# Performance work log

Hardware: AMD Instinct MI355X
Metric: run time of the kernel (lower is better)

## Reference

```python
import jax, jax.numpy as jnp
import numpy as np

B, C, H, W = 2, 128, 64, 64


def setup_inputs() -> dict:
    key = jax.random.key(0)
    ks = jax.random.split(key, 16)
    s = 1.0 / np.sqrt(C)
    d = {
        "x": jax.random.normal(ks[0], (B, C, H, W), jnp.float32),
        "y": jax.random.normal(ks[1], (B, C, H, W), jnp.float32),
    }
    names = ["qr", "qi", "kr", "ki", "vr", "vi"]
    for i, n in enumerate(names):
        d["W" + n] = jax.random.normal(ks[2 + 2 * i], (C, C), jnp.float32) * s
        d["b" + n] = jax.random.normal(ks[3 + 2 * i], (C,), jnp.float32) * s
    return d


def _lin(t, Wt, bt):
    # t: [b, n, c]; torch Linear: t @ W^T + b
    return jnp.einsum("bnc,dc->bnd", t, Wt) + bt


def reference(x, y, Wqr, bqr, Wqi, bqi, Wkr, bkr, Wki, bki, Wvr, bvr, Wvi, bvi):
    b, c, h, w = x.shape
    xf = jnp.fft.fft2(x)  # over last two axes (h, w)
    yf = jnp.fft.fft2(y)
    # b c h w -> b (h w) c
    def flat(t):
        return t.transpose(0, 2, 3, 1).reshape(b, h * w, c)
    xr, xi = flat(xf.real), flat(xf.imag)
    yr, yi = flat(yf.real), flat(yf.imag)

    Qr = _lin(xr, Wqr, bqr) - _lin(xi, Wqi, bqi)
    Qi = _lin(xi, Wqr, bqr) + _lin(xr, Wqi, bqi)
    Kr = _lin(yr, Wkr, bkr) - _lin(yi, Wki, bki)
    Ki = _lin(yi, Wkr, bkr) + _lin(yr, Wki, bki)
    Vr = _lin(yr, Wvr, bvr) - _lin(yi, Wvi, bvi)
    Vi = _lin(yi, Wvr, bvr) + _lin(yr, Wvi, bvi)

    sr = jnp.einsum("bnc,bmc->bnm", Qr, Kr) - jnp.einsum("bnc,bmc->bnm", Qi, Ki)
    si = jnp.einsum("bnc,bmc->bnm", Qr, Ki) + jnp.einsum("bnc,bmc->bnm", Qi, Kr)
    scores = jnp.sqrt(sr * sr + si * si + 1e-8)
    attn = jax.nn.softmax(scores, axis=-1)

    out_r = jnp.einsum("bnm,bmc->bnc", attn, Vr)
    out_i = jnp.einsum("bnm,bmc->bnc", attn, Vi)
    out_c = jax.lax.complex(out_r, out_i)
    # b (h w) c -> b c h w
    out_c = out_c.reshape(b, h, w, c).transpose(0, 3, 1, 2)
    return jnp.fft.ifft2(out_c).real
```

## Files before the change

kernel.cpp:

```cpp
#include <hip/hip_runtime.h>
#include <math.h>


#define PI2 6.283185307179586f

typedef __attribute__((ext_vector_type(8))) short short8;
typedef __attribute__((ext_vector_type(4))) float f32x4;

#define MFMA16(A,B,C) __builtin_amdgcn_mfma_f32_16x16x32_bf16((A),(B),(C),0,0,0)

__device__ inline unsigned short f2bf(float x){
  union{float f; unsigned int u;} a; a.f = x;
  unsigned int r = (a.u + 0x7fffu + ((a.u>>16)&1u)) >> 16;
  return (unsigned short)r;
}
__device__ inline float bf2f(unsigned short h){
  union{unsigned int u; float f;} a; a.u = ((unsigned int)h)<<16; return a.f;
}
__device__ inline short8 neg8(short8 x){
  union{short8 v; unsigned int u[4];} a; a.v = x;
  a.u[0]^=0x80008000u; a.u[1]^=0x80008000u; a.u[2]^=0x80008000u; a.u[3]^=0x80008000u;
  return a.v;
}
__device__ inline void gload_lds16(const void* g, void* lds){
  __builtin_amdgcn_global_load_lds((const __attribute__((address_space(1))) unsigned int*)g,
                                   (__attribute__((address_space(3))) unsigned int*)lds,
                                   16, 0, 0);
}

__global__ __launch_bounds__(256) void dft2_fwd_kernel(
    const float* __restrict__ x, const float* __restrict__ y,
    float* __restrict__ xr, float* __restrict__ xi,
    float* __restrict__ yr, float* __restrict__ yi)
{
  __shared__ float Xs[4096];
  __shared__ float Tr[4096], Ti[4096];
  __shared__ float twc[64], tws[64];
  int blk = blockIdx.x;
  const float* src; float *outr, *outi;
  int plane;
  if (blk < 256) { src = x; outr = xr; outi = xi; plane = blk; }
  else           { src = y; outr = yr; outi = yi; plane = blk - 256; }
  int b = plane >> 7, c = plane & 127;
  int t = threadIdx.x;
  if (t < 64) {
    float ang = -PI2 * (float)t / 64.0f;
    twc[t] = cosf(ang); tws[t] = sinf(ang);
  }
  const float* p = src + ((size_t)plane << 12);
  for (int i = t; i < 4096; i += 256) Xs[i] = p[i];
  __syncthreads();
  for (int j = 0; j < 16; j++) {
    int o = t + 256 * j; int h = o >> 6, wp = o & 63;
    float ar = 0.f, ai = 0.f;
    for (int w = 0; w < 64; w++) {
      int k = (w * wp) & 63;
      float v = Xs[h * 64 + w];
      ar = fmaf(v, twc[k], ar);
      ai = fmaf(v, tws[k], ai);
    }
    Tr[h * 64 + wp] = ar; Ti[h * 64 + wp] = ai;
  }
  __syncthreads();
  size_t ob = ((size_t)b * 4096) * 128 + c;
  for (int j = 0; j < 16; j++) {
    int o = t + 256 * j; int hp = o >> 6, wp = o & 63;
    float ar = 0.f, ai = 0.f;
    for (int h = 0; h < 64; h++) {
      int k = (h * hp) & 63;
      float cr = twc[k], ci = tws[k];
      float tr = Tr[h * 64 + wp], ti = Ti[h * 64 + wp];
      ar += tr * cr - ti * ci;
      ai += tr * ci + ti * cr;
    }
    int n = (hp << 6) + wp;
    outr[ob + (size_t)n * 128] = ar;
    outi[ob + (size_t)n * 128] = ai;
  }
}

__global__ __launch_bounds__(256) void proj_kernel(
    const float* __restrict__ xr, const float* __restrict__ xi,
    const float* __restrict__ yr, const float* __restrict__ yi,
    const float* __restrict__ Wqr, const float* __restrict__ bqr,
    const float* __restrict__ Wqi, const float* __restrict__ bqi,
    const float* __restrict__ Wkr, const float* __restrict__ bkr,
    const float* __restrict__ Wki, const float* __restrict__ bki,
    const float* __restrict__ Wvr, const float* __restrict__ bvr,
    const float* __restrict__ Wvi, const float* __restrict__ bvi,
    unsigned short* __restrict__ FQ, unsigned short* __restrict__ FK,
    unsigned short* __restrict__ FV)
{
  __shared__ float Asr[64 * 33], Asi[64 * 33], Wsr[128 * 33], Wsi[128 * 33];
  int nt = blockIdx.x, lin = blockIdx.y, b = blockIdx.z;
  const float *ar, *ai, *Wr, *Wi, *br_, *bi_;
  unsigned short* F;
  if (lin == 0)      { ar = xr; ai = xi; Wr = Wqr; Wi = Wqi; br_ = bqr; bi_ = bqi; F = FQ; }
  else if (lin == 1) { ar = yr; ai = yi; Wr = Wkr; Wi = Wki; br_ = bkr; bi_ = bki; F = FK; }
  else               { ar = yr; ai = yi; Wr = Wvr; Wi = Wvi; br_ = bvr; bi_ = bvi; F = FV; }
  int t = threadIdx.x; int td = t & 15, tn = t >> 4;
  int n0 = nt * 64;
  size_t abase = (size_t)b * 4096 * 128 + (size_t)n0 * 128;
  const size_t PS = (size_t)2 * 4096 * 128;
  float accr[4][8] = {}, acci[4][8] = {};
  for (int kk = 0; kk < 4; kk++) {
    __syncthreads();
    for (int idx = t; idx < 64 * 32; idx += 256) {
      int r = idx >> 5, ccol = idx & 31;
      Asr[r * 33 + ccol] = ar[abase + (size_t)r * 128 + kk * 32 + ccol];
      Asi[r * 33 + ccol] = ai[abase + (size_t)r * 128 + kk * 32 + ccol];
    }
    for (int idx = t; idx < 128 * 32; idx += 256) {
      int r = idx >> 5, ccol = idx & 31;
      Wsr[r * 33 + ccol] = Wr[(size_t)r * 128 + kk * 32 + ccol];
      Wsi[r * 33 + ccol] = Wi[(size_t)r * 128 + kk * 32 + ccol];
    }
    __syncthreads();
    for (int k = 0; k < 32; k++) {
      float a_r[4], a_i[4], w_r[8], w_i[8];
      #pragma unroll
      for (int i = 0; i < 4; i++) {
        a_r[i] = Asr[(tn * 4 + i) * 33 + k];
        a_i[i] = Asi[(tn * 4 + i) * 33 + k];
      }
      #pragma unroll
      for (int jj = 0; jj < 8; jj++) {
        w_r[jj] = Wsr[(td + 16 * jj) * 33 + k];
        w_i[jj] = Wsi[(td + 16 * jj) * 33 + k];
      }
      #pragma unroll
      for (int i = 0; i < 4; i++)
        #pragma unroll
        for (int jj = 0; jj < 8; jj++) {
          accr[i][jj] += a_r[i] * w_r[jj] - a_i[i] * w_i[jj];
          acci[i][jj] += a_i[i] * w_r[jj] + a_r[i] * w_i[jj];
        }
    }
  }
  for (int jj = 0; jj < 8; jj++) {
    int d = td + 16 * jj;
    float brd = br_[d], bid = bi_[d];
    #pragma unroll
    for (int i = 0; i < 4; i++) {
      int n = n0 + tn * 4 + i;
      float cr = accr[i][jj] + (brd - bid);
      float ci = acci[i][jj] + (brd + bid);
      size_t base = ((size_t)b * 4096 + n) * 128 + d;
      if (lin <= 1) {
        unsigned short rh = f2bf(cr); unsigned short rl = f2bf(cr - bf2f(rh));
        unsigned short ih = f2bf(ci); unsigned short il = f2bf(ci - bf2f(ih));
        F[0 * PS + base] = rh;
        F[1 * PS + base] = rl;
        F[2 * PS + base] = ih;
        F[3 * PS + base] = il;
      } else {
        F[0 * PS + base] = f2bf(cr);
        F[1 * PS + base] = f2bf(ci);
      }
    }
  }
}

__global__ __launch_bounds__(256) void kpack_kernel(
    const unsigned short* __restrict__ F, unsigned short* __restrict__ Kpk)
{
  int blk = blockIdx.x;
  int b = blk >> 6, mt = blk & 63;
  int t = threadIdx.x;
  size_t obase = (size_t)blk * 4096;
  #pragma unroll
  for (int k = 0; k < 16; k++) {
    int idx = t + 256 * k;
    int l = idx & 63, s = (idx >> 6) & 3, tml = (idx >> 8) & 3, a = idx >> 10;
    int n = mt * 64 + tml * 16 + (l & 15);
    int c0 = 32 * s + 8 * (l >> 4);
    const short8 v = *(const short8*)(F + (((size_t)(a * 2 + b) * 4096 + n) * 128 + c0));
    *(short8*)(Kpk + (obase + idx) * 8) = v;
  }
}

__global__ __launch_bounds__(256) void vpack_kernel(
    const unsigned short* __restrict__ F, unsigned short* __restrict__ Vpk)
{
  __shared__ unsigned short Vs[2 * 32 * 128];
  int blk = blockIdx.x;
  int b = blk >> 7, sm = blk & 127;
  int t = threadIdx.x;
  const size_t PS = (size_t)2 * 4096 * 128;
  #pragma unroll
  for (int p = 0; p < 2; p++) {
    #pragma unroll
    for (int k = 0; k < 2; k++) {
      int idx8 = t + 256 * k;
      int nn = idx8 >> 4, d0 = (idx8 & 15) * 8;
      const short8 v = *(const short8*)(F + p * PS + ((size_t)(b * 4096 + sm * 32 + nn)) * 128 + d0);
      *(short8*)(Vs + (p * 32 + nn) * 128 + d0) = v;
    }
  }
  __syncthreads();
  size_t obase = (size_t)blk * 1024;
  #pragma unroll
  for (int k = 0; k < 4; k++) {
    int idx = t + 256 * k;
    int lv = idx & 63, tc = idx >> 6;
    int vh = tc >> 3;
    int d = (tc & 7) * 16 + (lv & 15);
    int nb = (lv >> 4) * 8;
    short8 v;
    #pragma unroll
    for (int j = 0; j < 8; j++)
      v[j] = (short)Vs[(vh * 32 + nb + j) * 128 + d];
    *(short8*)(Vpk + (obase + idx) * 8) = v;
  }
}

__global__ __launch_bounds__(256, 2) void attn_mfma_kernel(
    const unsigned short* __restrict__ FQ, const short* __restrict__ Kpk,
    const short* __restrict__ Vpk,
    float* __restrict__ Or_, float* __restrict__ Oi_)
{
  __shared__ __align__(16) short Klds[32768];
  __shared__ __align__(16) short Pfrag[16 * 72];
  __shared__ __align__(16) float rmax[16][4];

  const int bi = blockIdx.x;
  const int xg = bi & 7;
  const int b = xg >> 2;
  const int qt2 = (bi >> 3) * 4 + (xg & 3);
  const int t = threadIdx.x;
  const int ms = t >> 6, l = t & 63;
  const int g = l >> 4, c = l & 15;

  const size_t PS = (size_t)2 * 4096 * 128;
  short8 Qf[4][4];
  #pragma unroll
  for (int a = 0; a < 4; a++)
    #pragma unroll
    for (int s = 0; s < 4; s++)
      Qf[a][s] = *(const short8*)(FQ + (size_t)a * PS +
                 ((size_t)(b * 4096) + qt2 * 16 + c) * 128 + 32 * s + 8 * g);

  f32x4 O[4], Oe;
  #pragma unroll
  for (int nt = 0; nt < 4; nt++) O[nt] = (f32x4){0.f, 0.f, 0.f, 0.f};
  Oe = (f32x4){0.f, 0.f, 0.f, 0.f};
  float Mq = -3e38f, escPrev = 1.0f;
  short8 Vreg[2][4];
  const short b1 = (short)0x3F80;
  const short8 ones = {b1, b1, b1, b1, b1, b1, b1, b1};
  const short8* Vp8 = (const short8*)Vpk;

  auto STAGE = [&](int tile) {
    const char* gsrc = (const char*)Kpk + ((size_t)(b * 64 + tile) << 16);
    #pragma unroll
    for (int i2 = 0; i2 < 16; i2++) {
      int ch = ms * 16 + i2;
      gload_lds16(gsrc + ch * 1024 + l * 16, (char*)Klds + ch * 1024);
    }
  };

  STAGE(0);
  asm volatile("s_waitcnt vmcnt(0)" ::: "memory");
  __builtin_amdgcn_s_barrier();
  __builtin_amdgcn_sched_barrier(0);

  f32x4 s0;
  for (int mt = 0; mt < 64; mt++) {
    if (mt > 0) {
      f32x4 esc4;
      #pragma unroll
      for (int r = 0; r < 4; r++) esc4[r] = __shfl(escPrev, 4 * g + r);
      #pragma unroll
      for (int r = 0; r < 4; r++) {
        #pragma unroll
        for (int nt = 0; nt < 4; nt++) O[nt][r] *= esc4[r];
        Oe[r] *= esc4[r];
      }
      __builtin_amdgcn_s_setprio(1);
      #pragma unroll
      for (int ks = 0; ks < 2; ks++) {
        short8 Pa = *(const short8*)&Pfrag[c * 72 + 32 * ks + 8 * g];
        #pragma unroll
        for (int nt = 0; nt < 4; nt++)
          O[nt] = MFMA16(Pa, Vreg[ks][nt], O[nt]);
        Oe = MFMA16(Pa, ones, Oe);
      }
      __builtin_amdgcn_s_setprio(0);
    }
    const short8* kb8 = (const short8*)Klds;
    f32x4 sr = (f32x4){0, 0, 0, 0}, si = (f32x4){0, 0, 0, 0};
    __builtin_amdgcn_s_setprio(1);
    #pragma unroll
    for (int s = 0; s < 4; s++) {
      short8 Arh = kb8[((0 * 4 + ms) * 4 + s) * 64 + l];
      short8 Arl = kb8[((1 * 4 + ms) * 4 + s) * 64 + l];
      short8 Aih = kb8[((2 * 4 + ms) * 4 + s) * 64 + l];
      short8 Ail = kb8[((3 * 4 + ms) * 4 + s) * 64 + l];
      short8 nqh = neg8(Qf[2][s]);
      short8 nql = neg8(Qf[3][s]);
      sr = MFMA16(Arh, Qf[0][s], sr);
      si = MFMA16(Arh, Qf[2][s], si);
      sr = MFMA16(Arh, Qf[1][s], sr);
      si = MFMA16(Arh, Qf[3][s], si);
      sr = MFMA16(Arl, Qf[0][s], sr);
      si = MFMA16(Arl, Qf[2][s], si);
      sr = MFMA16(Aih, nqh, sr);
      si = MFMA16(Aih, Qf[0][s], si);
      sr = MFMA16(Aih, nql, sr);
      si = MFMA16(Aih, Qf[1][s], si);
      sr = MFMA16(Ail, nqh, sr);
      si = MFMA16(Ail, Qf[0][s], si);
    }
    __builtin_amdgcn_s_setprio(0);
    #pragma unroll
    for (int r = 0; r < 4; r++)
      s0[r] = sqrtf(sr[r] * sr[r] + si[r] * si[r] + 1e-8f);
    float mloc = fmaxf(fmaxf(s0[0], s0[1]), fmaxf(s0[2], s0[3]));
    mloc = fmaxf(mloc, __shfl_xor(mloc, 16));
    mloc = fmaxf(mloc, __shfl_xor(mloc, 32));
    if (l < 16) rmax[l][ms] = mloc;
    asm volatile("s_waitcnt lgkmcnt(0)" ::: "memory");
    __builtin_amdgcn_s_barrier();
    __builtin_amdgcn_sched_barrier(0);
    if (mt + 1 < 64) STAGE(mt + 1);
    {
      f32x4 rm4 = *(const f32x4*)&rmax[c][0];
      float Mnew = fmaxf(fmaxf(rm4[0], rm4[1]), fmaxf(rm4[2], rm4[3]));
      Mnew = fmaxf(Mq, Mnew);
      escPrev = __expf(Mq - Mnew);
      Mq = Mnew;
      f32x4 p;
      #pragma unroll
      for (int r = 0; r < 4; r++) p[r] = __expf(s0[r] - Mnew);
      unsigned int* pw = (unsigned int*)&Pfrag[c * 72 + 16 * ms + 4 * g];
      pw[0] = (unsigned int)f2bf(p[0]) | ((unsigned int)f2bf(p[1]) << 16);
      pw[1] = (unsigned int)f2bf(p[2]) | ((unsigned int)f2bf(p[3]) << 16);
      #pragma unroll
      for (int ks = 0; ks < 2; ks++)
        #pragma unroll
        for (int nt = 0; nt < 4; nt++)
          Vreg[ks][nt] = Vp8[((size_t)((b * 128 + mt * 2 + ks) * 16 + ms * 4 + nt)) * 64 + l];
    }
    __builtin_amdgcn_sched_barrier(0);
    asm volatile("s_waitcnt vmcnt(8) lgkmcnt(0)" ::: "memory");
    __builtin_amdgcn_s_barrier();
    __builtin_amdgcn_sched_barrier(0);
  }
  {
    f32x4 esc4;
    #pragma unroll
    for (int r = 0; r < 4; r++) esc4[r] = __shfl(escPrev, 4 * g + r);
    #pragma unroll
    for (int r = 0; r < 4; r++) {
      #pragma unroll
      for (int nt = 0; nt < 4; nt++) O[nt][r] *= esc4[r];
      Oe[r] *= esc4[r];
    }
    #pragma unroll
    for (int ks = 0; ks < 2; ks++) {
      short8 Pa = *(const short8*)&Pfrag[c * 72 + 32 * ks + 8 * g];
      #pragma unroll
      for (int nt = 0; nt < 4; nt++)
        O[nt] = MFMA16(Pa, Vreg[ks][nt], O[nt]);
      Oe = MFMA16(Pa, ones, Oe);
    }
  }
  const size_t base = (size_t)b * 4096 * 128;
  f32x4 inv;
  #pragma unroll
  for (int r = 0; r < 4; r++) inv[r] = 1.0f / Oe[r];
  #pragma unroll
  for (int nt = 0; nt < 4; nt++) {
    int cc = ms * 64 + nt * 16 + c;
    #pragma unroll
    for (int r = 0; r < 4; r++) {
      int row = qt2 * 16 + 4 * g + r;
      float v = O[nt][r] * inv[r];
      if (cc < 128) Or_[base + (size_t)row * 128 + cc] = v;
      else          Oi_[base + (size_t)row * 128 + cc - 128] = v;
    }
  }
}

__global__ __launch_bounds__(256) void idft2_kernel(
    const float* __restrict__ Or_, const float* __restrict__ Oi_,
    float* __restrict__ out)
{
  __shared__ float Ar[4096], Ai[4096], Tr[4096], Ti[4096];
  __shared__ float twc[64], tws[64];
  int plane = blockIdx.x; int b = plane >> 7, c = plane & 127;
  int t = threadIdx.x;
  if (t < 64) {
    float ang = PI2 * (float)t / 64.0f;
    twc[t] = cosf(ang); tws[t] = sinf(ang);
  }
  size_t ibase = (size_t)b * 4096 * 128 + c;
  for (int i = t; i < 4096; i += 256) {
    Ar[i] = Or_[ibase + (size_t)i * 128];
    Ai[i] = Oi_[ibase + (size_t)i * 128];
  }
  __syncthreads();
  for (int j = 0; j < 16; j++) {
    int o = t + 256 * j; int hp = o >> 6, w = o & 63;
    float tr = 0.f, ti = 0.f;
    for (int wp = 0; wp < 64; wp++) {
      int k = (wp * w) & 63;
      float cr = twc[k], ci = tws[k];
      float ar = Ar[hp * 64 + wp], ai = Ai[hp * 64 + wp];
      tr += ar * cr - ai * ci;
      ti += ai * cr + ar * ci;
    }
    Tr[hp * 64 + w] = tr; Ti[hp * 64 + w] = ti;
  }
  __syncthreads();
  size_t obase = ((size_t)plane) << 12;
  for (int j = 0; j < 16; j++) {
    int o = t + 256 * j; int h = o >> 6, w = o & 63;
    float acc = 0.f;
    for (int hp = 0; hp < 64; hp++) {
      int k = (hp * h) & 63;
      acc += Tr[hp * 64 + w] * twc[k] - Ti[hp * 64 + w] * tws[k];
    }
    out[obase + o] = acc * (1.0f / 4096.0f);
  }
}

extern "C" void kernel_launch(void* const* d_in, const int* in_sizes, int n_in,
                              void* d_out, int out_size, void* d_ws, size_t ws_size,
                              hipStream_t stream) {
  const float* x   = (const float*)d_in[0];
  const float* y   = (const float*)d_in[1];
  const float* Wqr = (const float*)d_in[2];  const float* bqr = (const float*)d_in[3];
  const float* Wqi = (const float*)d_in[4];  const float* bqi = (const float*)d_in[5];
  const float* Wkr = (const float*)d_in[6];  const float* bkr = (const float*)d_in[7];
  const float* Wki = (const float*)d_in[8];  const float* bki = (const float*)d_in[9];
  const float* Wvr = (const float*)d_in[10]; const float* bvr = (const float*)d_in[11];
  const float* Wvi = (const float*)d_in[12]; const float* bvi = (const float*)d_in[13];
  char* wsb = (char*)d_ws;
  if (ws_size < ((size_t)40 << 20)) return;
  unsigned short* FQ  = (unsigned short*)(wsb);
  unsigned short* FK  = (unsigned short*)(wsb + ((size_t)8  << 20));
  unsigned short* FV  = (unsigned short*)(wsb + ((size_t)16 << 20));
  float* xr = (float*)(wsb + ((size_t)20 << 20));
  float* xi = (float*)(wsb + ((size_t)24 << 20));
  float* yr = (float*)(wsb + ((size_t)28 << 20));
  float* yi = (float*)(wsb + ((size_t)32 << 20));
  unsigned short* Kpk = (unsigned short*)(wsb + ((size_t)28 << 20));
  unsigned short* Vpk = (unsigned short*)(wsb + ((size_t)36 << 20));
  float* Or_ = (float*)(wsb + ((size_t)20 << 20));
  float* Oi_ = (float*)(wsb + ((size_t)24 << 20));
  float* out = (float*)d_out;

  hipLaunchKernelGGL(dft2_fwd_kernel, dim3(512), dim3(256), 0, stream,
                     x, y, xr, xi, yr, yi);
  hipLaunchKernelGGL(proj_kernel, dim3(64, 3, 2), dim3(256), 0, stream,
                     xr, xi, yr, yi,
                     Wqr, bqr, Wqi, bqi, Wkr, bkr, Wki, bki, Wvr, bvr, Wvi, bvi,
                     FQ, FK, FV);
  hipLaunchKernelGGL(kpack_kernel, dim3(128), dim3(256), 0, stream, FK, Kpk);
  hipLaunchKernelGGL(vpack_kernel, dim3(256), dim3(256), 0, stream, FV, Vpk);
  hipLaunchKernelGGL(attn_mfma_kernel, dim3(512), dim3(256), 0, stream,
                     FQ, (const short*)Kpk, (const short*)Vpk, Or_, Oi_);
  hipLaunchKernelGGL(idft2_kernel, dim3(256), dim3(256), 0, stream,
                     Or_, Oi_, out);
}
```

Before: 406.5 us.

## Split attention keys across waves with per-wave online softmax and LDS merge

The attention kernel now gives each wave its own subset of key tiles, with its own online softmax and a full 256-column output accumulator, in place of having the four waves cooperate on each shared K tile through LDS staging and barriers every iteration. Partial results are merged at the end through LDS using per-wave max and sum rescaling. K fragments are read directly from global memory, so the kpack kernel and async LDS staging are dropped. This removes the per-tile barriers and the extra pack launch. In exchange it raises register pressure (64 accumulator floats per lane), turns K reads into uncached-by-LDS global loads, and adds a serialized reduction at the end.

After: 527.8 us. 29.8% more time.

```diff
diff --git a/kernel.cpp b/kernel.cpp
--- a/kernel.cpp
+++ b/kernel.cpp
@@ -21,11 +21,6 @@
   union{short8 v; unsigned int u[4];} a; a.v = x;
   a.u[0]^=0x80008000u; a.u[1]^=0x80008000u; a.u[2]^=0x80008000u; a.u[3]^=0x80008000u;
   return a.v;
-}
-__device__ inline void gload_lds16(const void* g, void* lds){
-  __builtin_amdgcn_global_load_lds((const __attribute__((address_space(1))) unsigned int*)g,
-                                   (__attribute__((address_space(3))) unsigned int*)lds,
-                                   16, 0, 0);
 }
 
 __global__ __launch_bounds__(256) void dft2_fwd_kernel(
@@ -161,24 +156,6 @@
   }
 }
 
-__global__ __launch_bounds__(256) void kpack_kernel(
-    const unsigned short* __restrict__ F, unsigned short* __restrict__ Kpk)
-{
-  int blk = blockIdx.x;
-  int b = blk >> 6, mt = blk & 63;
-  int t = threadIdx.x;
-  size_t obase = (size_t)blk * 4096;
-  #pragma unroll
-  for (int k = 0; k < 16; k++) {
-    int idx = t + 256 * k;
-    int l = idx & 63, s = (idx >> 6) & 3, tml = (idx >> 8) & 3, a = idx >> 10;
-    int n = mt * 64 + tml * 16 + (l & 15);
-    int c0 = 32 * s + 8 * (l >> 4);
-    const short8 v = *(const short8*)(F + (((size_t)(a * 2 + b) * 4096 + n) * 128 + c0));
-    *(short8*)(Kpk + (obase + idx) * 8) = v;
-  }
-}
-
 __global__ __launch_bounds__(256) void vpack_kernel(
     const unsigned short* __restrict__ F, unsigned short* __restrict__ Vpk)
 {
@@ -215,20 +192,21 @@
 }
 
 __global__ __launch_bounds__(256, 2) void attn_mfma_kernel(
-    const unsigned short* __restrict__ FQ, const short* __restrict__ Kpk,
+    const unsigned short* __restrict__ FQ, const unsigned short* __restrict__ FK,
     const short* __restrict__ Vpk,
     float* __restrict__ Or_, float* __restrict__ Oi_)
 {
-  __shared__ __align__(16) short Klds[32768];
-  __shared__ __align__(16) short Pfrag[16 * 72];
-  __shared__ __align__(16) float rmax[16][4];
+  __shared__ __align__(16) short Ppriv[4][16 * 72];
+  __shared__ __align__(16) float Oacc[16 * 256];
+  __shared__ float Msh[4][16];
+  __shared__ float Lsh[4][16];
 
   const int bi = blockIdx.x;
   const int xg = bi & 7;
   const int b = xg >> 2;
   const int qt2 = (bi >> 3) * 4 + (xg & 3);
   const int t = threadIdx.x;
-  const int ms = t >> 6, l = t & 63;
+  const int w = t >> 6, l = t & 63;
   const int g = l >> 4, c = l & 15;
 
   const size_t PS = (size_t)2 * 4096 * 128;
@@ -240,145 +218,130 @@
       Qf[a][s] = *(const short8*)(FQ + (size_t)a * PS +
                  ((size_t)(b * 4096) + qt2 * 16 + c) * 128 + 32 * s + 8 * g);
 
-  f32x4 O[4], Oe;
-  #pragma unroll
-  for (int nt = 0; nt < 4; nt++) O[nt] = (f32x4){0.f, 0.f, 0.f, 0.f};
+  f32x4 O[16], Oe;
+  #pragma unroll
+  for (int tc = 0; tc < 16; tc++) O[tc] = (f32x4){0.f, 0.f, 0.f, 0.f};
   Oe = (f32x4){0.f, 0.f, 0.f, 0.f};
-  float Mq = -3e38f, escPrev = 1.0f;
-  short8 Vreg[2][4];
+  float Mq = -3e38f;
   const short b1 = (short)0x3F80;
   const short8 ones = {b1, b1, b1, b1, b1, b1, b1, b1};
   const short8* Vp8 = (const short8*)Vpk;
 
-  auto STAGE = [&](int tile) {
-    const char* gsrc = (const char*)Kpk + ((size_t)(b * 64 + tile) << 16);
-    #pragma unroll
-    for (int i2 = 0; i2 < 16; i2++) {
-      int ch = ms * 16 + i2;
-      gload_lds16(gsrc + ch * 1024 + l * 16, (char*)Klds + ch * 1024);
-    }
-  };
-
-  STAGE(0);
-  asm volatile("s_waitcnt vmcnt(0)" ::: "memory");
-  __builtin_amdgcn_s_barrier();
-  __builtin_amdgcn_sched_barrier(0);
-
-  f32x4 s0;
-  for (int mt = 0; mt < 64; mt++) {
-    if (mt > 0) {
-      f32x4 esc4;
-      #pragma unroll
-      for (int r = 0; r < 4; r++) esc4[r] = __shfl(escPrev, 4 * g + r);
-      #pragma unroll
-      for (int r = 0; r < 4; r++) {
+  for (int ti = 0; ti < 16; ti++) {
+    const int tile = ti * 4 + w;
+    float mags[4][4];
+    #pragma unroll
+    for (int sub = 0; sub < 4; sub++) {
+      f32x4 sr = (f32x4){0, 0, 0, 0}, si = (f32x4){0, 0, 0, 0};
+      #pragma unroll
+      for (int s = 0; s < 4; s++) {
+        const unsigned short* kb = FK +
+            ((size_t)(b * 4096) + tile * 64 + sub * 16 + c) * 128 + 32 * s + 8 * g;
+        short8 Arh = *(const short8*)(kb);
+        short8 Arl = *(const short8*)(kb + PS);
+        short8 Aih = *(const short8*)(kb + 2 * PS);
+        short8 Ail = *(const short8*)(kb + 3 * PS);
+        short8 nqh = neg8(Qf[2][s]);
+        short8 nql = neg8(Qf[3][s]);
+        sr = MFMA16(Arh, Qf[0][s], sr);
+        si = MFMA16(Arh, Qf[2][s], si);
+        sr = MFMA16(Arh, Qf[1][s], sr);
+        si = MFMA16(Arh, Qf[3][s], si);
+        sr = MFMA16(Arl, Qf[0][s], sr);
+        si = MFMA16(Arl, Qf[2][s], si);
+        sr = MFMA16(Aih, nqh, sr);
+        si = MFMA16(Aih, Qf[0][s], si);
+        sr = MFMA16(Aih, nql, sr);
+        si = MFMA16(Aih, Qf[1][s], si);
+        sr = MFMA16(Ail, nqh, sr);
+        si = MFMA16(Ail, Qf[0][s], si);
+      }
+      #pragma unroll
+      for (int r = 0; r < 4; r++)
+        mags[sub][r] = sqrtf(sr[r] * sr[r] + si[r] * si[r] + 1e-8f);
+    }
+    float mloc = -3e38f;
+    #pragma unroll
+    for (int sub = 0; sub < 4; sub++)
+      #pragma unroll
+      for (int r = 0; r < 4; r++) mloc = fmaxf(mloc, mags[sub][r]);
+    mloc = fmaxf(mloc, __shfl_xor(mloc, 16));
+    mloc = fmaxf(mloc, __shfl_xor(mloc, 32));
+    float Mnew = fmaxf(Mq, mloc);
+    float esc = __expf(Mq - Mnew);
+    Mq = Mnew;
+    #pragma unroll
+    for (int sub = 0; sub < 4; sub++) {
+      float p0 = __expf(mags[sub][0] - Mnew);
+      float p1 = __expf(mags[sub][1] - Mnew);
+      float p2 = __expf(mags[sub][2] - Mnew);
+      float p3 = __expf(mags[sub][3] - Mnew);
+      unsigned int* pw = (unsigned int*)&Ppriv[w][c * 72 + sub * 16 + 4 * g];
+      pw[0] = (unsigned int)f2bf(p0) | ((unsigned int)f2bf(p1) << 16);
+      pw[1] = (unsigned int)f2bf(p2) | ((unsigned int)f2bf(p3) << 16);
+    }
+    f32x4 esc4;
+    #pragma unroll
+    for (int r = 0; r < 4; r++) esc4[r] = __shfl(esc, 4 * g + r);
+    #pragma unroll
+    for (int tc = 0; tc < 16; tc++)
+      #pragma unroll
+      for (int r = 0; r < 4; r++) O[tc][r] *= esc4[r];
+    #pragma unroll
+    for (int r = 0; r < 4; r++) Oe[r] *= esc4[r];
+    #pragma unroll
+    for (int kk = 0; kk < 2; kk++) {
+      short8 PA = *(const short8*)&Ppriv[w][c * 72 + kk * 32 + 8 * g];
+      const int sm = tile * 2 + kk;
+      const size_t vb = ((size_t)((b * 128 + sm) * 16)) * 64 + l;
+      #pragma unroll
+      for (int h = 0; h < 4; h++) {
+        short8 VB[4];
         #pragma unroll
-        for (int nt = 0; nt < 4; nt++) O[nt][r] *= esc4[r];
-        Oe[r] *= esc4[r];
-      }
-      __builtin_amdgcn_s_setprio(1);
-      #pragma unroll
-      for (int ks = 0; ks < 2; ks++) {
-        short8 Pa = *(const short8*)&Pfrag[c * 72 + 32 * ks + 8 * g];
+        for (int nt = 0; nt < 4; nt++) VB[nt] = Vp8[vb + (size_t)(h * 4 + nt) * 64];
         #pragma unroll
         for (int nt = 0; nt < 4; nt++)
-          O[nt] = MFMA16(Pa, Vreg[ks][nt], O[nt]);
-        Oe = MFMA16(Pa, ones, Oe);
+          O[h * 4 + nt] = MFMA16(PA, VB[nt], O[h * 4 + nt]);
       }
-      __builtin_amdgcn_s_setprio(0);
-    }
-    const short8* kb8 = (const short8*)Klds;
-    f32x4 sr = (f32x4){0, 0, 0, 0}, si = (f32x4){0, 0, 0, 0};
-    __builtin_amdgcn_s_setprio(1);
-    #pragma unroll
-    for (int s = 0; s < 4; s++) {
-      short8 Arh = kb8[((0 * 4 + ms) * 4 + s) * 64 + l];
-      short8 Arl = kb8[((1 * 4 + ms) * 4 + s) * 64 + l];
-      short8 Aih = kb8[((2 * 4 + ms) * 4 + s) * 64 + l];
-      short8 Ail = kb8[((3 * 4 + ms) * 4 + s) * 64 + l];
-      short8 nqh = neg8(Qf[2][s]);
-      short8 nql = neg8(Qf[3][s]);
-      sr = MFMA16(Arh, Qf[0][s], sr);
-      si = MFMA16(Arh, Qf[2][s], si);
-      sr = MFMA16(Arh, Qf[1][s], sr);
-      si = MFMA16(Arh, Qf[3][s], si);
-      sr = MFMA16(Arl, Qf[0][s], sr);
-      si = MFMA16(Arl, Qf[2][s], si);
-      sr = MFMA16(Aih, nqh, sr);
-      si = MFMA16(Aih, Qf[0][s], si);
-      sr = MFMA16(Aih, nql, sr);
-      si = MFMA16(Aih, Qf[1][s], si);
-      sr = MFMA16(Ail, nqh, sr);
-      si = MFMA16(Ail, Qf[0][s], si);
-    }
-    __builtin_amdgcn_s_setprio(0);
-    #pragma unroll
-    for (int r = 0; r < 4; r++)
-      s0[r] = sqrtf(sr[r] * sr[r] + si[r] * si[r] + 1e-8f);
-    float mloc = fmaxf(fmaxf(s0[0], s0[1]), fmaxf(s0[2], s0[3]));
-    mloc = fmaxf(mloc, __shfl_xor(mloc, 16));
-    mloc = fmaxf(mloc, __shfl_xor(mloc, 32));
-    if (l < 16) rmax[l][ms] = mloc;
-    asm volatile("s_waitcnt lgkmcnt(0)" ::: "memory");
-    __builtin_amdgcn_s_barrier();
-    __builtin_amdgcn_sched_barrier(0);
-    if (mt + 1 < 64) STAGE(mt + 1);
-    {
-      f32x4 rm4 = *(const f32x4*)&rmax[c][0];
-      float Mnew = fmaxf(fmaxf(rm4[0], rm4[1]), fmaxf(rm4[2], rm4[3]));
-      Mnew = fmaxf(Mq, Mnew);
-      escPrev = __expf(Mq - Mnew);
-      Mq = Mnew;
-      f32x4 p;
-      #pragma unroll
-      for (int r = 0; r < 4; r++) p[r] = __expf(s0[r] - Mnew);
-      unsigned int* pw = (unsigned int*)&Pfrag[c * 72 + 16 * ms + 4 * g];
-      pw[0] = (unsigned int)f2bf(p[0]) | ((unsigned int)f2bf(p[1]) << 16);
-      pw[1] = (unsigned int)f2bf(p[2]) | ((unsigned int)f2bf(p[3]) << 16);
-      #pragma unroll
-      for (int ks = 0; ks < 2; ks++)
+      Oe = MFMA16(PA, ones, Oe);
+    }
+  }
+
+  if (l < 16) Msh[w][l] = Mq;
+  __syncthreads();
+  float escw[4];
+  #pragma unroll
+  for (int r = 0; r < 4; r++) {
+    int q = 4 * g + r;
+    float mstar = fmaxf(fmaxf(Msh[0][q], Msh[1][q]), fmaxf(Msh[2][q], Msh[3][q]));
+    escw[r] = __expf(Msh[w][q] - mstar);
+  }
+  if (c == 0) {
+    #pragma unroll
+    for (int r = 0; r < 4; r++) Lsh[w][4 * g + r] = Oe[r] * escw[r];
+  }
+  for (int round = 0; round < 4; round++) {
+    if (w == round) {
+      #pragma unroll
+      for (int tc = 0; tc < 16; tc++)
         #pragma unroll
-        for (int nt = 0; nt < 4; nt++)
-          Vreg[ks][nt] = Vp8[((size_t)((b * 128 + mt * 2 + ks) * 16 + ms * 4 + nt)) * 64 + l];
-    }
-    __builtin_amdgcn_sched_barrier(0);
-    asm volatile("s_waitcnt vmcnt(8) lgkmcnt(0)" ::: "memory");
-    __builtin_amdgcn_s_barrier();
-    __builtin_amdgcn_sched_barrier(0);
-  }
-  {
-    f32x4 esc4;
-    #pragma unroll
-    for (int r = 0; r < 4; r++) esc4[r] = __shfl(escPrev, 4 * g + r);
-    #pragma unroll
-    for (int r = 0; r < 4; r++) {
-      #pragma unroll
-      for (int nt = 0; nt < 4; nt++) O[nt][r] *= esc4[r];
-      Oe[r] *= esc4[r];
-    }
-    #pragma unroll
-    for (int ks = 0; ks < 2; ks++) {
-      short8 Pa = *(const short8*)&Pfrag[c * 72 + 32 * ks + 8 * g];
-      #pragma unroll
-      for (int nt = 0; nt < 4; nt++)
-        O[nt] = MFMA16(Pa, Vreg[ks][nt], O[nt]);
-      Oe = MFMA16(Pa, ones, Oe);
-    }
+        for (int r = 0; r < 4; r++) {
+          int idx = (4 * g + r) * 256 + tc * 16 + c;
+          float v = O[tc][r] * escw[r];
+          if (round == 0) Oacc[idx] = v; else Oacc[idx] += v;
+        }
+    }
+    __syncthreads();
   }
   const size_t base = (size_t)b * 4096 * 128;
-  f32x4 inv;
-  #pragma unroll
-  for (int r = 0; r < 4; r++) inv[r] = 1.0f / Oe[r];
-  #pragma unroll
-  for (int nt = 0; nt < 4; nt++) {
-    int cc = ms * 64 + nt * 16 + c;
-    #pragma unroll
-    for (int r = 0; r < 4; r++) {
-      int row = qt2 * 16 + 4 * g + r;
-      float v = O[nt][r] * inv[r];
-      if (cc < 128) Or_[base + (size_t)row * 128 + cc] = v;
-      else          Oi_[base + (size_t)row * 128 + cc - 128] = v;
-    }
+  const int col = w * 64 + l;
+  #pragma unroll
+  for (int q = 0; q < 16; q++) {
+    float Lq = Lsh[0][q] + Lsh[1][q] + Lsh[2][q] + Lsh[3][q];
+    float v = Oacc[q * 256 + col] / Lq;
+    int row = qt2 * 16 + q;
+    if (col < 128) Or_[base + (size_t)row * 128 + col] = v;
+    else           Oi_[base + (size_t)row * 128 + col - 128] = v;
   }
 }
 
@@ -445,7 +408,6 @@
   float* xi = (float*)(wsb + ((size_t)24 << 20));
   float* yr = (float*)(wsb + ((size_t)28 << 20));
   float* yi = (float*)(wsb + ((size_t)32 << 20));
-  unsigned short* Kpk = (unsigned short*)(wsb + ((size_t)28 << 20));
   unsigned short* Vpk = (unsigned short*)(wsb + ((size_t)36 << 20));
   float* Or_ = (float*)(wsb + ((size_t)20 << 20));
   float* Oi_ = (float*)(wsb + ((size_t)24 << 20));
@@ -457,10 +419,9 @@
                      xr, xi, yr, yi,
                      Wqr, bqr, Wqi, bqi, Wkr, bkr, Wki, bki, Wvr, bvr, Wvi, bvi,
                      FQ, FK, FV);
-  hipLaunchKernelGGL(kpack_kernel, dim3(128), dim3(256), 0, stream, FK, Kpk);
   hipLaunchKernelGGL(vpack_kernel, dim3(256), dim3(256), 0, stream, FV, Vpk);
   hipLaunchKernelGGL(attn_mfma_kernel, dim3(512), dim3(256), 0, stream,
-                     FQ, (const short*)Kpk, (const short*)Vpk, Or_, Oi_);
+                     FQ, FK, (const short*)Vpk, Or_, Oi_);
   hipLaunchKernelGGL(idft2_kernel, dim3(256), dim3(256), 0, stream,
                      Or_, Oi_, out);
 }
```
